# Kernel tuning notes

Measured on AMD Instinct MI355X. Metric: run time of the kernel, lower is better.

The kernel has to match this reference:

```python
import jax, jax.numpy as jnp
import numpy as np

N, D, E = 100000, 128, 1600000
BN_EPS = 1e-5

def setup_inputs() -> dict:
    key = jax.random.key(0)
    k1, k2, k3 = jax.random.split(key, 3)
    src_embeddings = jax.random.normal(k1, (N, D), dtype=jnp.float32)
    dst_embeddings = jax.random.normal(k2, (N, D), dtype=jnp.float32)
    graph = jax.random.randint(k3, (2, E), 0, N, dtype=jnp.int64)
    bn_weight = jnp.ones((1,), dtype=jnp.float32)
    bn_bias = jnp.zeros((1,), dtype=jnp.float32)
    return {
        "src_embeddings": src_embeddings,
        "dst_embeddings": dst_embeddings,
        "graph": graph,
        "bn_weight": bn_weight,
        "bn_bias": bn_bias,
    }

def reference(src_embeddings, dst_embeddings, graph, bn_weight, bn_bias):
    # gather endpoint embeddings by edge indices: [E, D]
    src = src_embeddings[graph[0]]
    dst = dst_embeddings[graph[1]]
    # squared distance per edge, clamped as in torch .clamp(min=1e-12)
    d2 = jnp.clip(jnp.sum((src - dst) ** 2, axis=-1), 1e-12, None)  # [E]
    likelihood = -jnp.log(d2)
    # BatchNorm1d(1) in training mode: batch mean, biased variance, eps=1e-5
    mu = jnp.mean(likelihood)
    var = jnp.mean((likelihood - mu) ** 2)
    edge_weights_logits = bn_weight[0] * (likelihood - mu) * jax.lax.rsqrt(var + BN_EPS) + bn_bias[0]
    # weighting_function = torch.sigmoid
    edge_weights = jax.nn.sigmoid(edge_weights_logits)
    # normalize=True: divide by mean
    edge_weights = edge_weights / jnp.mean(edge_weights)
    edge_weights = edge_weights[:, None]  # [E, 1]
    return graph, edge_weights, edge_weights_logits
```

## Files before the change

### kernel.cpp

```cpp
#include <hip/hip_runtime.h>
#include <math.h>

#define EMB_D 128
#define BN_EPS 1e-5f
#define GATHER_BLOCKS 2048
#define OVF_CAP 8192

typedef float v2f __attribute__((ext_vector_type(2)));

#if defined(__has_builtin)
#if __has_builtin(__builtin_amdgcn_cvt_pk_f32_fp8) && __has_builtin(__builtin_amdgcn_cvt_pk_fp8_f32)
#define FP8_HW 1
#endif
#endif

__device__ __forceinline__ unsigned int sw_f32_to_fp8(float x) {
    unsigned int u = __float_as_uint(x);
    unsigned int s = u >> 31;
    int e = (int)((u >> 23) & 0xff) - 127;
    unsigned int m = u & 0x7fffff;
    m += 0x7FFFF + ((m >> 20) & 1);
    if (m >> 23) { m = 0; e += 1; }
    int e8 = e + 7;
    if (e8 <= 0) return s << 7;
    if (e8 >= 15) return (s << 7) | 0x7E;
    return (s << 7) | ((unsigned)e8 << 3) | (m >> 20);
}

__device__ __forceinline__ float sw_fp8_to_f32(unsigned int v) {
    unsigned int s = (v >> 7) & 1, e = (v >> 3) & 15, m = v & 7;
    if (e == 0) return 0.0f;
    unsigned int bits = (s << 31) | ((e - 7 + 127) << 23) | (m << 20);
    return __uint_as_float(bits);
}

__device__ __forceinline__ unsigned int pack4_fp8(float4 v) {
#ifdef FP8_HW
    unsigned int o = 0;
    o = (unsigned int)__builtin_amdgcn_cvt_pk_fp8_f32(v.x, v.y, (int)o, false);
    o = (unsigned int)__builtin_amdgcn_cvt_pk_fp8_f32(v.z, v.w, (int)o, true);
    return o;
#else
    return sw_f32_to_fp8(v.x) | (sw_f32_to_fp8(v.y) << 8) |
           (sw_f32_to_fp8(v.z) << 16) | (sw_f32_to_fp8(v.w) << 24);
#endif
}

__device__ __forceinline__ float fp8x4_d2(unsigned int ua, unsigned int ub) {
#ifdef FP8_HW
    v2f a0 = __builtin_amdgcn_cvt_pk_f32_fp8((int)ua, false);
    v2f a1 = __builtin_amdgcn_cvt_pk_f32_fp8((int)ua, true);
    v2f b0 = __builtin_amdgcn_cvt_pk_f32_fp8((int)ub, false);
    v2f b1 = __builtin_amdgcn_cvt_pk_f32_fp8((int)ub, true);
    float dx = a0.x - b0.x, dy = a0.y - b0.y;
    float dz = a1.x - b1.x, dw = a1.y - b1.y;
#else
    float dx = sw_fp8_to_f32(ua & 0xff)         - sw_fp8_to_f32(ub & 0xff);
    float dy = sw_fp8_to_f32((ua >> 8) & 0xff)  - sw_fp8_to_f32((ub >> 8) & 0xff);
    float dz = sw_fp8_to_f32((ua >> 16) & 0xff) - sw_fp8_to_f32((ub >> 16) & 0xff);
    float dw = sw_fp8_to_f32(ua >> 24)          - sw_fp8_to_f32(ub >> 24);
#endif
    return fmaf(dx, dx, fmaf(dy, dy, fmaf(dz, dz, dw * dw)));
}

__device__ __forceinline__ float chunk_d2(uint4 a, uint4 b) {
    return fp8x4_d2(a.x, b.x) + fp8x4_d2(a.y, b.y)
         + fp8x4_d2(a.z, b.z) + fp8x4_d2(a.w, b.w);
}

__device__ __forceinline__ float edge_L(const unsigned char* src8,
                                        const unsigned char* dst8,
                                        int s, int d, int sub) {
    const uint4* sa = (const uint4*)(src8 + (long long)s * 128) + sub * 4;
    const uint4* sb = (const uint4*)(dst8 + (long long)d * 128) + sub * 4;
    const uint4 a0 = sa[0], a1 = sa[1], a2 = sa[2], a3 = sa[3];
    const uint4 b0 = sb[0], b1 = sb[1], b2 = sb[2], b3 = sb[3];
    float p = chunk_d2(a0, b0) + chunk_d2(a1, b1)
            + chunk_d2(a2, b2) + chunk_d2(a3, b3);
    p += __shfl_xor(p, 1, 64);
    return -logf(fmaxf(p, 1e-12f));
}

__global__ void prep_kernel(const float* __restrict__ src,
                            const float* __restrict__ dst,
                            unsigned int* __restrict__ src8,
                            unsigned int* __restrict__ dst8,
                            long long nElem,
                            double* __restrict__ acc,
                            unsigned int* __restrict__ cursors,
                            unsigned int cap)
{
    if (blockIdx.x == 0) {
        if (threadIdx.x < 65) cursors[threadIdx.x] = threadIdx.x * cap;
        if (threadIdx.x >= 65 && threadIdx.x < 68) acc[threadIdx.x - 65] = 0.0;
    }
    const long long nthreads = (long long)gridDim.x * blockDim.x;
    const long long tid0 = (long long)blockIdx.x * blockDim.x + threadIdx.x;
    const long long nvec = nElem / 4;
    for (long long i = tid0; i < nvec; i += nthreads)
        src8[i] = pack4_fp8(((const float4*)src)[i]);
    for (long long i = tid0; i < nvec; i += nthreads)
        dst8[i] = pack4_fp8(((const float4*)dst)[i]);
}

__global__ void bin_kernel(const int* __restrict__ g,
                           long long E,
                           unsigned long long* __restrict__ rec,
                           unsigned int* __restrict__ cursors,
                           unsigned int cap,
                           float inv_slice)
{
    __shared__ unsigned int hist[64];
    __shared__ unsigned int curs[64];

    const long long chunkSz = (long long)blockDim.x * 8;
    const long long nchunks = (E + chunkSz - 1) / chunkSz;

    for (long long c = blockIdx.x; c < nchunks; c += gridDim.x) {
        const long long base = c * chunkSz;
        if (threadIdx.x < 64) hist[threadIdx.x] = 0;
        __syncthreads();

        int bb[8];
        unsigned long long pk[8];
        #pragma unroll
        for (int k = 0; k < 8; ++k) {
            const long long e = base + (long long)k * blockDim.x + threadIdx.x;
            bb[k] = -1;
            if (e < E) {
                const unsigned int s = (unsigned int)g[e];
                const unsigned int d = (unsigned int)g[E + e];
                int bs = (int)((float)s * inv_slice); bs = bs > 7 ? 7 : bs;
                int bd = (int)((float)d * inv_slice); bd = bd > 7 ? 7 : bd;
                bb[k] = bs * 8 + bd;
                pk[k] = (unsigned long long)s | ((unsigned long long)d << 20)
                      | ((unsigned long long)e << 40);
                atomicAdd(&hist[bb[k]], 1u);
            }
        }
        __syncthreads();
        if (threadIdx.x < 64 && hist[threadIdx.x] > 0)
            curs[threadIdx.x] = atomicAdd(&cursors[threadIdx.x], hist[threadIdx.x]);
        __syncthreads();

        #pragma unroll
        for (int k = 0; k < 8; ++k) {
            if (bb[k] >= 0) {
                unsigned int off = atomicAdd(&curs[bb[k]], 1u);
                const unsigned int lim = (unsigned int)(bb[k] + 1) * cap;
                if (off < lim) {
                    rec[off] = pk[k];
                } else {
                    unsigned int oo = atomicAdd(&cursors[64], 1u);
                    if (oo < 64u * cap + OVF_CAP) rec[oo] = pk[k];
                }
            }
        }
        __syncthreads();
    }
}

__global__ void edge_l_binned_kernel(const unsigned char* __restrict__ src8,
                                     const unsigned char* __restrict__ dst8,
                                     const unsigned long long* __restrict__ rec,
                                     const unsigned int* __restrict__ cursors,
                                     unsigned int cap,
                                     float* __restrict__ l_out,
                                     double* __restrict__ acc)
{
    const int sub = threadIdx.x & 1;
    const int eg  = threadIdx.x >> 1;
    const int xcd = blockIdx.x & 7;
    const int local = blockIdx.x >> 3;
    const unsigned int perXcd = gridDim.x >> 3;
    const unsigned int stride = perXcd * 128;

    double sumL = 0.0, sumL2 = 0.0;

    for (int j = 0; j < 8; ++j) {
        const int b = xcd * 8 + j;
        const unsigned int start = (unsigned int)b * cap;
        unsigned int end = cursors[b];
        const unsigned int lim = (unsigned int)(b + 1) * cap;
        if (end > lim) end = lim;
        for (unsigned int idx = start + (unsigned int)local * 128u + eg;
             idx < end; idx += stride) {
            const unsigned long long v = rec[idx];
            const int s = (int)(v & 0xFFFFFu);
            const int d = (int)((v >> 20) & 0xFFFFFu);
            const long long eid = (long long)(v >> 40);
            const float L = edge_L(src8, dst8, s, d, sub);
            if (sub == 0) {
                l_out[eid] = L;
                sumL  += (double)L;
                sumL2 += (double)L * (double)L;
            }
        }
    }

    {
        const unsigned int start = 64u * cap;
        unsigned int end = cursors[64];
        if (end > start + OVF_CAP) end = start + OVF_CAP;
        const unsigned int gstride = gridDim.x * 128u;
        for (unsigned int idx = start + blockIdx.x * 128u + eg;
             idx < end; idx += gstride) {
            const unsigned long long v = rec[idx];
            const int s = (int)(v & 0xFFFFFu);
            const int d = (int)((v >> 20) & 0xFFFFFu);
            const long long eid = (long long)(v >> 40);
            const float L = edge_L(src8, dst8, s, d, sub);
            if (sub == 0) {
                l_out[eid] = L;
                sumL  += (double)L;
                sumL2 += (double)L * (double)L;
            }
        }
    }

    __shared__ double sA[256];
    __shared__ double sB[256];
    sA[threadIdx.x] = sumL;
    sB[threadIdx.x] = sumL2;
    __syncthreads();
    for (int ofs = 128; ofs >= 1; ofs >>= 1) {
        if ((int)threadIdx.x < ofs) {
            sA[threadIdx.x] += sA[threadIdx.x + ofs];
            sB[threadIdx.x] += sB[threadIdx.x + ofs];
        }
        __syncthreads();
    }
    if (threadIdx.x == 0) {
        atomicAdd(&acc[0], sA[0]);
        atomicAdd(&acc[1], sB[0]);
    }
}

__global__ void edge_l_fp8_kernel(const unsigned char* __restrict__ src8,
                                  const unsigned char* __restrict__ dst8,
                                  const int* __restrict__ g,
                                  long long E,
                                  float*  __restrict__ l_out,
                                  double* __restrict__ acc)
{
    const int sub = threadIdx.x & 1;
    const int eg  = threadIdx.x >> 1;
    const long long stride = (long long)gridDim.x * 128;

    double sumL = 0.0, sumL2 = 0.0;

    long long e = (long long)blockIdx.x * 128 + eg;
    int s = 0, d = 0;
    if (e < E) { s = g[e]; d = g[E + e]; }

    while (e < E) {
        const long long en = e + stride;
        int sn = 0, dn = 0;
        if (en < E) { sn = g[en]; dn = g[E + en]; }
        const float L = edge_L(src8, dst8, s, d, sub);
        if (sub == 0) {
            l_out[e] = L;
            sumL  += (double)L;
            sumL2 += (double)L * (double)L;
        }
        e = en; s = sn; d = dn;
    }

    __shared__ double sA[256];
    __shared__ double sB[256];
    sA[threadIdx.x] = sumL;
    sB[threadIdx.x] = sumL2;
    __syncthreads();
    for (int ofs = 128; ofs >= 1; ofs >>= 1) {
        if ((int)threadIdx.x < ofs) {
            sA[threadIdx.x] += sA[threadIdx.x + ofs];
            sB[threadIdx.x] += sB[threadIdx.x + ofs];
        }
        __syncthreads();
    }
    if (threadIdx.x == 0) {
        atomicAdd(&acc[0], sA[0]);
        atomicAdd(&acc[1], sB[0]);
    }
}

__global__ void edge_l_kernel(const float* __restrict__ src,
                              const float* __restrict__ dst,
                              const int*   __restrict__ g,
                              long long E,
                              float*  __restrict__ l_out,
                              double* __restrict__ acc)
{
    const int sub  = threadIdx.x & 7;
    const int egrp = threadIdx.x >> 3;
    const long long stride = (long long)gridDim.x * 32;

    double sumL = 0.0, sumL2 = 0.0;

    long long e = (long long)blockIdx.x * 32 + egrp;
    int s = 0, d = 0;
    if (e < E) { s = g[e]; d = g[E + e]; }

    while (e < E) {
        const long long en = e + stride;
        int sn = 0, dn = 0;
        if (en < E) { sn = g[en]; dn = g[E + en]; }

        const float4* sa = (const float4*)(src + (long long)s * EMB_D);
        const float4* sb = (const float4*)(dst + (long long)d * EMB_D);
        const float4 a0 = sa[sub];      const float4 b0 = sb[sub];
        const float4 a1 = sa[sub + 8];  const float4 b1 = sb[sub + 8];
        const float4 a2 = sa[sub + 16]; const float4 b2 = sb[sub + 16];
        const float4 a3 = sa[sub + 24]; const float4 b3 = sb[sub + 24];

        float dx, dy, dz, dw, p = 0.f;
        dx = a0.x-b0.x; dy = a0.y-b0.y; dz = a0.z-b0.z; dw = a0.w-b0.w;
        p += fmaf(dx,dx,fmaf(dy,dy,fmaf(dz,dz,dw*dw)));
        dx = a1.x-b1.x; dy = a1.y-b1.y; dz = a1.z-b1.z; dw = a1.w-b1.w;
        p += fmaf(dx,dx,fmaf(dy,dy,fmaf(dz,dz,dw*dw)));
        dx = a2.x-b2.x; dy = a2.y-b2.y; dz = a2.z-b2.z; dw = a2.w-b2.w;
        p += fmaf(dx,dx,fmaf(dy,dy,fmaf(dz,dz,dw*dw)));
        dx = a3.x-b3.x; dy = a3.y-b3.y; dz = a3.z-b3.z; dw = a3.w-b3.w;
        p += fmaf(dx,dx,fmaf(dy,dy,fmaf(dz,dz,dw*dw)));

        p += __shfl_xor(p, 1, 64);
        p += __shfl_xor(p, 2, 64);
        p += __shfl_xor(p, 4, 64);

        if (sub == 0) {
            const float L = -logf(fmaxf(p, 1e-12f));
            l_out[e] = L;
            sumL  += (double)L;
            sumL2 += (double)L * (double)L;
        }
        e = en; s = sn; d = dn;
    }

    __shared__ double sA[256];
    __shared__ double sB[256];
    sA[threadIdx.x] = sumL;
    sB[threadIdx.x] = sumL2;
    __syncthreads();
    for (int ofs = 128; ofs >= 1; ofs >>= 1) {
        if ((int)threadIdx.x < ofs) {
            sA[threadIdx.x] += sA[threadIdx.x + ofs];
            sB[threadIdx.x] += sB[threadIdx.x + ofs];
        }
        __syncthreads();
    }
    if (threadIdx.x == 0) {
        atomicAdd(&acc[0], sA[0]);
        atomicAdd(&acc[1], sB[0]);
    }
}

__global__ void bn_sig_kernel(float* __restrict__ logits,
                              float* __restrict__ ew,
                              const double* __restrict__ acc,
                              double* __restrict__ sig_acc,
                              const float* __restrict__ bn_w,
                              const float* __restrict__ bn_b,
                              long long E)
{
    const long long nthreads = (long long)gridDim.x * blockDim.x;
    const long long tid0 = (long long)blockIdx.x * blockDim.x + threadIdx.x;

    __shared__ float s_mu, s_inv, s_w, s_b;
    if (threadIdx.x == 0) {
        const double mu  = acc[0] / (double)E;
        const double var = acc[1] / (double)E - mu * mu;
        s_mu  = (float)mu;
        s_inv = (float)(1.0 / sqrt(var + (double)BN_EPS));
        s_w   = bn_w[0];
        s_b   = bn_b[0];
    }
    __syncthreads();
    const float mu = s_mu, inv = s_inv, w = s_w, b = s_b;

    double sig = 0.0;
    for (long long i = tid0; i < E; i += nthreads) {
        const float L = logits[i];
        const float z = w * (L - mu) * inv + b;
        logits[i] = z;
        const float sg = 1.0f / (1.0f + expf(-z));
        ew[i] = sg;
        sig += (double)sg;
    }

    __shared__ double sS[256];
    sS[threadIdx.x] = sig;
    __syncthreads();
    for (int ofs = 128; ofs >= 1; ofs >>= 1) {
        if ((int)threadIdx.x < ofs)
            sS[threadIdx.x] += sS[threadIdx.x + ofs];
        __syncthreads();
    }
    if (threadIdx.x == 0)
        atomicAdd(sig_acc, sS[0]);
}

__global__ void norm_graph_kernel(float* __restrict__ ew,
                                  const double* __restrict__ sig_acc,
                                  const int* __restrict__ g,
                                  float* __restrict__ out_graph,
                                  long long E)
{
    const long long nthreads = (long long)gridDim.x * blockDim.x;
    const long long tid0 = (long long)blockIdx.x * blockDim.x + threadIdx.x;
    const float scale = (float)((double)E / sig_acc[0]);

    const long long nvec = E / 4;
    for (long long i = tid0; i < nvec; i += nthreads) {
        float4 v = ((float4*)ew)[i];
        v.x *= scale; v.y *= scale; v.z *= scale; v.w *= scale;
        ((float4*)ew)[i] = v;
    }
    for (long long i = nvec * 4 + tid0; i < E; i += nthreads)
        ew[i] *= scale;

    const long long gvec = (2 * E) / 4;
    for (long long i = tid0; i < gvec; i += nthreads) {
        const int4 v = ((const int4*)g)[i];
        float4 f;
        f.x = (float)v.x; f.y = (float)v.y; f.z = (float)v.z; f.w = (float)v.w;
        ((float4*)out_graph)[i] = f;
    }
    for (long long i = gvec * 4 + tid0; i < 2 * E; i += nthreads)
        out_graph[i] = (float)g[i];
}

extern "C" void kernel_launch(void* const* d_in, const int* in_sizes, int n_in,
                              void* d_out, int out_size, void* d_ws, size_t ws_size,
                              hipStream_t stream) {
    const float* src  = (const float*)d_in[0];
    const float* dst  = (const float*)d_in[1];
    const int*   g    = (const int*)d_in[2];
    const float* bn_w = (const float*)d_in[3];
    const float* bn_b = (const float*)d_in[4];

    const long long N = (long long)in_sizes[0] / EMB_D;
    const long long E = (long long)in_sizes[2] / 2;

    float* out        = (float*)d_out;
    float* out_graph  = out;
    float* out_ew     = out + 2 * E;
    float* out_logits = out + 3 * E;

    double*       acc     = (double*)d_ws;
    unsigned int* cursors = (unsigned int*)((char*)d_ws + 64);
    unsigned char* src8   = (unsigned char*)d_ws + 512;
    unsigned char* dst8   = src8 + (size_t)N * EMB_D;
    unsigned long long* rec = (unsigned long long*)(dst8 + (size_t)N * EMB_D);

    const unsigned int cap = (unsigned int)(E / 64 + 2048);
    const size_t need_full = 512 + (size_t)N * EMB_D * 2
                           + ((size_t)64 * cap + OVF_CAP) * 8;
    const size_t need_fp8  = 512 + (size_t)N * EMB_D * 2;

    const int slice_sz = (int)((N + 7) / 8);
    const float inv_slice = 1.0f / (float)slice_sz;

    if (ws_size >= need_full && N < (1 << 20) && E < (1LL << 24)) {
        prep_kernel<<<4096, 256, 0, stream>>>(src, dst,
                                              (unsigned int*)src8,
                                              (unsigned int*)dst8,
                                              N * EMB_D, acc, cursors, cap);
        bin_kernel<<<1024, 256, 0, stream>>>(g, E, rec, cursors, cap, inv_slice);
        edge_l_binned_kernel<<<GATHER_BLOCKS, 256, 0, stream>>>(
            src8, dst8, rec, cursors, cap, out_logits, acc);
    } else if (ws_size >= need_fp8) {
        prep_kernel<<<4096, 256, 0, stream>>>(src, dst,
                                              (unsigned int*)src8,
                                              (unsigned int*)dst8,
                                              N * EMB_D, acc, cursors, cap);
        edge_l_fp8_kernel<<<4096, 256, 0, stream>>>(src8, dst8, g, E,
                                                    out_logits, acc);
    } else {
        hipMemsetAsync(d_ws, 0, 3 * sizeof(double), stream);
        edge_l_kernel<<<4096, 256, 0, stream>>>(src, dst, g, E, out_logits, acc);
    }

    bn_sig_kernel<<<2048, 256, 0, stream>>>(out_logits, out_ew, acc, &acc[2],
                                            bn_w, bn_b, E);
    norm_graph_kernel<<<2048, 256, 0, stream>>>(out_ew, &acc[2], g, out_graph, E);
}
```

Baseline: 293.8 us.

## Fuse prep with binning, regroup gather to 8 lanes, vectorize BN pass

Merges the fp8 table conversion and the edge binning into one kernel that also writes the float graph output, so the norm kernel skips the graph copy. Bin cursors become relative counts and are zeroed by a memset instead of in-kernel initialization. The gather kernel walks each XCD's bins through a single flat index, uses 8 lanes per edge with two edges in flight per lane group, and writes logits with nontemporal stores. The BN/sigmoid pass is vectorized with float4, and grid sizes for the tail kernels are halved. The gain in parallelism and fewer launches comes with a prefix lookup per record, and the fused prep kernel depends on the binning grid being suitable for the conversion loop.

```diff
diff --git a/kernel.cpp b/kernel.cpp
--- a/kernel.cpp
+++ b/kernel.cpp
@@ -81,35 +81,42 @@
     return -logf(fmaxf(p, 1e-12f));
 }
 
-__global__ void prep_kernel(const float* __restrict__ src,
-                            const float* __restrict__ dst,
-                            unsigned int* __restrict__ src8,
-                            unsigned int* __restrict__ dst8,
-                            long long nElem,
-                            double* __restrict__ acc,
-                            unsigned int* __restrict__ cursors,
-                            unsigned int cap)
-{
-    if (blockIdx.x == 0) {
-        if (threadIdx.x < 65) cursors[threadIdx.x] = threadIdx.x * cap;
-        if (threadIdx.x >= 65 && threadIdx.x < 68) acc[threadIdx.x - 65] = 0.0;
-    }
-    const long long nthreads = (long long)gridDim.x * blockDim.x;
-    const long long tid0 = (long long)blockIdx.x * blockDim.x + threadIdx.x;
-    const long long nvec = nElem / 4;
-    for (long long i = tid0; i < nvec; i += nthreads)
-        src8[i] = pack4_fp8(((const float4*)src)[i]);
-    for (long long i = tid0; i < nvec; i += nthreads)
-        dst8[i] = pack4_fp8(((const float4*)dst)[i]);
-}
-
-__global__ void bin_kernel(const int* __restrict__ g,
-                           long long E,
-                           unsigned long long* __restrict__ rec,
-                           unsigned int* __restrict__ cursors,
-                           unsigned int cap,
-                           float inv_slice)
-{
+__device__ __forceinline__ unsigned int flat_to_rec(unsigned int f,
+                                                    const unsigned int (&pre)[9],
+                                                    unsigned int cap) {
+    unsigned int j = 0, pj = 0;
+    #pragma unroll
+    for (int k = 1; k < 8; ++k) {
+        const bool ge = (f >= pre[k]);
+        j  = ge ? (unsigned int)k : j;
+        pj = ge ? pre[k] : pj;
+    }
+    return j * cap + (f - pj);
+}
+
+__global__ void prep_bin_kernel(const float* __restrict__ src,
+                                const float* __restrict__ dst,
+                                unsigned int* __restrict__ src8,
+                                unsigned int* __restrict__ dst8,
+                                long long nElem,
+                                const int* __restrict__ g,
+                                long long E,
+                                float* __restrict__ out_graph,
+                                unsigned long long* __restrict__ rec,
+                                unsigned int* __restrict__ cursors,
+                                unsigned int cap,
+                                float inv_slice)
+{
+    {
+        const long long nthreads = (long long)gridDim.x * blockDim.x;
+        const long long tid0 = (long long)blockIdx.x * blockDim.x + threadIdx.x;
+        const long long nvec = nElem / 4;
+        for (long long i = tid0; i < nvec; i += nthreads)
+            src8[i] = pack4_fp8(((const float4*)src)[i]);
+        for (long long i = tid0; i < nvec; i += nthreads)
+            dst8[i] = pack4_fp8(((const float4*)dst)[i]);
+    }
+
     __shared__ unsigned int hist[64];
     __shared__ unsigned int curs[64];
 
@@ -130,6 +137,8 @@
             if (e < E) {
                 const unsigned int s = (unsigned int)g[e];
                 const unsigned int d = (unsigned int)g[E + e];
+                out_graph[e]     = (float)s;
+                out_graph[E + e] = (float)d;
                 int bs = (int)((float)s * inv_slice); bs = bs > 7 ? 7 : bs;
                 int bd = (int)((float)d * inv_slice); bd = bd > 7 ? 7 : bd;
                 bb[k] = bs * 8 + bd;
@@ -147,12 +156,11 @@
         for (int k = 0; k < 8; ++k) {
             if (bb[k] >= 0) {
                 unsigned int off = atomicAdd(&curs[bb[k]], 1u);
-                const unsigned int lim = (unsigned int)(bb[k] + 1) * cap;
-                if (off < lim) {
-                    rec[off] = pk[k];
+                if (off < cap) {
+                    rec[(unsigned int)bb[k] * cap + off] = pk[k];
                 } else {
                     unsigned int oo = atomicAdd(&cursors[64], 1u);
-                    if (oo < 64u * cap + OVF_CAP) rec[oo] = pk[k];
+                    if (oo < OVF_CAP) rec[64u * cap + oo] = pk[k];
                 }
             }
         }
@@ -160,62 +168,169 @@
     }
 }
 
-__global__ void edge_l_binned_kernel(const unsigned char* __restrict__ src8,
-                                     const unsigned char* __restrict__ dst8,
-                                     const unsigned long long* __restrict__ rec,
-                                     const unsigned int* __restrict__ cursors,
-                                     unsigned int cap,
-                                     float* __restrict__ l_out,
-                                     double* __restrict__ acc)
-{
-    const int sub = threadIdx.x & 1;
-    const int eg  = threadIdx.x >> 1;
+__global__ void edge_l_binned2_kernel(const unsigned char* __restrict__ src8,
+                                      const unsigned char* __restrict__ dst8,
+                                      const unsigned long long* __restrict__ rec,
+                                      const unsigned int* __restrict__ cursors,
+                                      unsigned int cap,
+                                      float* __restrict__ l_out,
+                                      double* __restrict__ acc)
+{
+    const int tid = threadIdx.x;
+    const int sub = tid & 7;
+    const int grp = tid >> 3;
     const int xcd = blockIdx.x & 7;
-    const int local = blockIdx.x >> 3;
-    const unsigned int perXcd = gridDim.x >> 3;
-    const unsigned int stride = perXcd * 128;
+    const unsigned int local = blockIdx.x >> 3;
+    const unsigned int nloc  = gridDim.x >> 3;
+
+    unsigned int pre[9];
+    pre[0] = 0;
+    #pragma unroll
+    for (int j = 0; j < 8; ++j) {
+        unsigned int c = cursors[xcd * 8 + j];
+        if (c > cap) c = cap;
+        pre[j + 1] = pre[j] + c;
+    }
+    const unsigned int M = pre[8];
+    const unsigned long long recBase = (unsigned long long)(xcd * 8) * cap;
 
     double sumL = 0.0, sumL2 = 0.0;
 
-    for (int j = 0; j < 8; ++j) {
-        const int b = xcd * 8 + j;
-        const unsigned int start = (unsigned int)b * cap;
-        unsigned int end = cursors[b];
-        const unsigned int lim = (unsigned int)(b + 1) * cap;
-        if (end > lim) end = lim;
-        for (unsigned int idx = start + (unsigned int)local * 128u + eg;
-             idx < end; idx += stride) {
-            const unsigned long long v = rec[idx];
-            const int s = (int)(v & 0xFFFFFu);
-            const int d = (int)((v >> 20) & 0xFFFFFu);
-            const long long eid = (long long)(v >> 40);
-            const float L = edge_L(src8, dst8, s, d, sub);
-            if (sub == 0) {
-                l_out[eid] = L;
+    const unsigned int perBlock = 64;
+    const unsigned int stride = nloc * perBlock;
+
+    for (unsigned int f0 = local * perBlock; f0 < M; f0 += stride) {
+        const unsigned int f1 = f0 + (unsigned int)grp;
+        const unsigned int f2 = f1 + 32u;
+        const bool ok1 = f1 < M;
+        const bool ok2 = f2 < M;
+
+        unsigned long long v1 = 0ull, v2 = 0ull;
+        if (ok1) v1 = rec[recBase + flat_to_rec(f1, pre, cap)];
+        if (ok2) v2 = rec[recBase + flat_to_rec(f2, pre, cap)];
+
+        const int s1 = (int)(v1 & 0xFFFFFu);
+        const int d1 = (int)((v1 >> 20) & 0xFFFFFu);
+        const int s2 = (int)(v2 & 0xFFFFFu);
+        const int d2i = (int)((v2 >> 20) & 0xFFFFFu);
+
+        const uint4 A1 = ((const uint4*)(src8 + (long long)s1 * 128))[sub];
+        const uint4 B1 = ((const uint4*)(dst8 + (long long)d1 * 128))[sub];
+        const uint4 A2 = ((const uint4*)(src8 + (long long)s2 * 128))[sub];
+        const uint4 B2 = ((const uint4*)(dst8 + (long long)d2i * 128))[sub];
+
+        float p1 = chunk_d2(A1, B1);
+        float p2 = chunk_d2(A2, B2);
+
+        p1 += __shfl_xor(p1, 1, 64);
+        p1 += __shfl_xor(p1, 2, 64);
+        p1 += __shfl_xor(p1, 4, 64);
+        p2 += __shfl_xor(p2, 1, 64);
+        p2 += __shfl_xor(p2, 2, 64);
+        p2 += __shfl_xor(p2, 4, 64);
+
+        if (sub == 0) {
+            if (ok1) {
+                const float L = -logf(fmaxf(p1, 1e-12f));
+                __builtin_nontemporal_store(L, &l_out[(long long)(v1 >> 40)]);
                 sumL  += (double)L;
                 sumL2 += (double)L * (double)L;
             }
-        }
-    }
-
-    {
-        const unsigned int start = 64u * cap;
-        unsigned int end = cursors[64];
-        if (end > start + OVF_CAP) end = start + OVF_CAP;
-        const unsigned int gstride = gridDim.x * 128u;
-        for (unsigned int idx = start + blockIdx.x * 128u + eg;
-             idx < end; idx += gstride) {
-            const unsigned long long v = rec[idx];
-            const int s = (int)(v & 0xFFFFFu);
-            const int d = (int)((v >> 20) & 0xFFFFFu);
-            const long long eid = (long long)(v >> 40);
-            const float L = edge_L(src8, dst8, s, d, sub);
-            if (sub == 0) {
-                l_out[eid] = L;
+            if (ok2) {
+                const float L = -logf(fmaxf(p2, 1e-12f));
+                __builtin_nontemporal_store(L, &l_out[(long long)(v2 >> 40)]);
                 sumL  += (double)L;
                 sumL2 += (double)L * (double)L;
             }
         }
+    }
+
+    {
+        unsigned int ovfN = cursors[64];
+        if (ovfN > OVF_CAP) ovfN = OVF_CAP;
+        const unsigned long long obase = 64ull * cap;
+        const unsigned int gstride = gridDim.x * 32u;
+        for (unsigned int f = blockIdx.x * 32u + (unsigned int)grp;
+             f < ovfN; f += gstride) {
+            const unsigned long long v = rec[obase + f];
+            const int s = (int)(v & 0xFFFFFu);
+            const int d = (int)((v >> 20) & 0xFFFFFu);
+            const uint4 A = ((const uint4*)(src8 + (long long)s * 128))[sub];
+            const uint4 B = ((const uint4*)(dst8 + (long long)d * 128))[sub];
+            float p = chunk_d2(A, B);
+            p += __shfl_xor(p, 1, 64);
+            p += __shfl_xor(p, 2, 64);
+            p += __shfl_xor(p, 4, 64);
+            if (sub == 0) {
+                const float L = -logf(fmaxf(p, 1e-12f));
+                __builtin_nontemporal_store(L, &l_out[(long long)(v >> 40)]);
+                sumL  += (double)L;
+                sumL2 += (double)L * (double)L;
+            }
+        }
+    }
+
+    __shared__ double sA[256];
+    __shared__ double sB[256];
+    sA[tid] = sumL;
+    sB[tid] = sumL2;
+    __syncthreads();
+    for (int ofs = 128; ofs >= 1; ofs >>= 1) {
+        if (tid < ofs) {
+            sA[tid] += sA[tid + ofs];
+            sB[tid] += sB[tid + ofs];
+        }
+        __syncthreads();
+    }
+    if (tid == 0) {
+        atomicAdd(&acc[0], sA[0]);
+        atomicAdd(&acc[1], sB[0]);
+    }
+}
+
+__global__ void prep_tables_kernel(const float* __restrict__ src,
+                                   const float* __restrict__ dst,
+                                   unsigned int* __restrict__ src8,
+                                   unsigned int* __restrict__ dst8,
+                                   long long nElem)
+{
+    const long long nthreads = (long long)gridDim.x * blockDim.x;
+    const long long tid0 = (long long)blockIdx.x * blockDim.x + threadIdx.x;
+    const long long nvec = nElem / 4;
+    for (long long i = tid0; i < nvec; i += nthreads)
+        src8[i] = pack4_fp8(((const float4*)src)[i]);
+    for (long long i = tid0; i < nvec; i += nthreads)
+        dst8[i] = pack4_fp8(((const float4*)dst)[i]);
+}
+
+__global__ void edge_l_fp8_kernel(const unsigned char* __restrict__ src8,
+                                  const unsigned char* __restrict__ dst8,
+                                  const int* __restrict__ g,
+                                  long long E,
+                                  float*  __restrict__ l_out,
+                                  double* __restrict__ acc)
+{
+    const int sub = threadIdx.x & 1;
+    const int eg  = threadIdx.x >> 1;
+    const long long stride = (long long)gridDim.x * 128;
+
+    double sumL = 0.0, sumL2 = 0.0;
+
+    long long e = (long long)blockIdx.x * 128 + eg;
+    int s = 0, d = 0;
+    if (e < E) { s = g[e]; d = g[E + e]; }
+
+    while (e < E) {
+        const long long en = e + stride;
+        int sn = 0, dn = 0;
+        if (en < E) { sn = g[en]; dn = g[E + en]; }
+        const float L = edge_L(src8, dst8, s, d, sub);
+        if (sub == 0) {
+            l_out[e] = L;
+            sumL  += (double)L;
+            sumL2 += (double)L * (double)L;
+        }
+        e = en; s = sn; d = dn;
     }
 
     __shared__ double sA[256];
@@ -236,20 +351,20 @@
     }
 }
 
-__global__ void edge_l_fp8_kernel(const unsigned char* __restrict__ src8,
-                                  const unsigned char* __restrict__ dst8,
-                                  const int* __restrict__ g,
-                                  long long E,
-                                  float*  __restrict__ l_out,
-                                  double* __restrict__ acc)
-{
-    const int sub = threadIdx.x & 1;
-    const int eg  = threadIdx.x >> 1;
-    const long long stride = (long long)gridDim.x * 128;
+__global__ void edge_l_kernel(const float* __restrict__ src,
+                              const float* __restrict__ dst,
+                              const int*   __restrict__ g,
+                              long long E,
+                              float*  __restrict__ l_out,
+                              double* __restrict__ acc)
+{
+    const int sub  = threadIdx.x & 7;
+    const int egrp = threadIdx.x >> 3;
+    const long long stride = (long long)gridDim.x * 32;
 
     double sumL = 0.0, sumL2 = 0.0;
 
-    long long e = (long long)blockIdx.x * 128 + eg;
+    long long e = (long long)blockIdx.x * 32 + egrp;
     int s = 0, d = 0;
     if (e < E) { s = g[e]; d = g[E + e]; }
 
@@ -257,8 +372,30 @@
         const long long en = e + stride;
         int sn = 0, dn = 0;
         if (en < E) { sn = g[en]; dn = g[E + en]; }
-        const float L = edge_L(src8, dst8, s, d, sub);
+
+        const float4* sa = (const float4*)(src + (long long)s * EMB_D);
+        const float4* sb = (const float4*)(dst + (long long)d * EMB_D);
+        const float4 a0 = sa[sub];      const float4 b0 = sb[sub];
+        const float4 a1 = sa[sub + 8];  const float4 b1 = sb[sub + 8];
+        const float4 a2 = sa[sub + 16]; const float4 b2 = sb[sub + 16];
+        const float4 a3 = sa[sub + 24]; const float4 b3 = sb[sub + 24];
+
+        float dx, dy, dz, dw, p = 0.f;
+        dx = a0.x-b0.x; dy = a0.y-b0.y; dz = a0.z-b0.z; dw = a0.w-b0.w;
+        p += fmaf(dx,dx,fmaf(dy,dy,fmaf(dz,dz,dw*dw)));
+        dx = a1.x-b1.x; dy = a1.y-b1.y; dz = a1.z-b1.z; dw = a1.w-b1.w;
+        p += fmaf(dx,dx,fmaf(dy,dy,fmaf(dz,dz,dw*dw)));
+        dx = a2.x-b2.x; dy = a2.y-b2.y; dz = a2.z-b2.z; dw = a2.w-b2.w;
+        p += fmaf(dx,dx,fmaf(dy,dy,fmaf(dz,dz,dw*dw)));
+        dx = a3.x-b3.x; dy = a3.y-b3.y; dz = a3.z-b3.z; dw = a3.w-b3.w;
+        p += fmaf(dx,dx,fmaf(dy,dy,fmaf(dz,dz,dw*dw)));
+
+        p += __shfl_xor(p, 1, 64);
+        p += __shfl_xor(p, 2, 64);
+        p += __shfl_xor(p, 4, 64);
+
         if (sub == 0) {
+            const float L = -logf(fmaxf(p, 1e-12f));
             l_out[e] = L;
             sumL  += (double)L;
             sumL2 += (double)L * (double)L;
@@ -284,76 +421,6 @@
     }
 }
 
-__global__ void edge_l_kernel(const float* __restrict__ src,
-                              const float* __restrict__ dst,
-                              const int*   __restrict__ g,
-                              long long E,
-                              float*  __restrict__ l_out,
-                              double* __restrict__ acc)
-{
-    const int sub  = threadIdx.x & 7;
-    const int egrp = threadIdx.x >> 3;
-    const long long stride = (long long)gridDim.x * 32;
-
-    double sumL = 0.0, sumL2 = 0.0;
-
-    long long e = (long long)blockIdx.x * 32 + egrp;
-    int s = 0, d = 0;
-    if (e < E) { s = g[e]; d = g[E + e]; }
-
-    while (e < E) {
-        const long long en = e + stride;
-        int sn = 0, dn = 0;
-        if (en < E) { sn = g[en]; dn = g[E + en]; }
-
-        const float4* sa = (const float4*)(src + (long long)s * EMB_D);
-        const float4* sb = (const float4*)(dst + (long long)d * EMB_D);
-        const float4 a0 = sa[sub];      const float4 b0 = sb[sub];
-        const float4 a1 = sa[sub + 8];  const float4 b1 = sb[sub + 8];
-        const float4 a2 = sa[sub + 16]; const float4 b2 = sb[sub + 16];
-        const float4 a3 = sa[sub + 24]; const float4 b3 = sb[sub + 24];
-
-        float dx, dy, dz, dw, p = 0.f;
-        dx = a0.x-b0.x; dy = a0.y-b0.y; dz = a0.z-b0.z; dw = a0.w-b0.w;
-        p += fmaf(dx,dx,fmaf(dy,dy,fmaf(dz,dz,dw*dw)));
-        dx = a1.x-b1.x; dy = a1.y-b1.y; dz = a1.z-b1.z; dw = a1.w-b1.w;
-        p += fmaf(dx,dx,fmaf(dy,dy,fmaf(dz,dz,dw*dw)));
-        dx = a2.x-b2.x; dy = a2.y-b2.y; dz = a2.z-b2.z; dw = a2.w-b2.w;
-        p += fmaf(dx,dx,fmaf(dy,dy,fmaf(dz,dz,dw*dw)));
-        dx = a3.x-b3.x; dy = a3.y-b3.y; dz = a3.z-b3.z; dw = a3.w-b3.w;
-        p += fmaf(dx,dx,fmaf(dy,dy,fmaf(dz,dz,dw*dw)));
-
-        p += __shfl_xor(p, 1, 64);
-        p += __shfl_xor(p, 2, 64);
-        p += __shfl_xor(p, 4, 64);
-
-        if (sub == 0) {
-            const float L = -logf(fmaxf(p, 1e-12f));
-            l_out[e] = L;
-            sumL  += (double)L;
-            sumL2 += (double)L * (double)L;
-        }
-        e = en; s = sn; d = dn;
-    }
-
-    __shared__ double sA[256];
-    __shared__ double sB[256];
-    sA[threadIdx.x] = sumL;
-    sB[threadIdx.x] = sumL2;
-    __syncthreads();
-    for (int ofs = 128; ofs >= 1; ofs >>= 1) {
-        if ((int)threadIdx.x < ofs) {
-            sA[threadIdx.x] += sA[threadIdx.x + ofs];
-            sB[threadIdx.x] += sB[threadIdx.x + ofs];
-        }
-        __syncthreads();
-    }
-    if (threadIdx.x == 0) {
-        atomicAdd(&acc[0], sA[0]);
-        atomicAdd(&acc[1], sB[0]);
-    }
-}
-
 __global__ void bn_sig_kernel(float* __restrict__ logits,
                               float* __restrict__ ew,
                               const double* __restrict__ acc,
@@ -378,7 +445,24 @@
     const float mu = s_mu, inv = s_inv, w = s_w, b = s_b;
 
     double sig = 0.0;
-    for (long long i = tid0; i < E; i += nthreads) {
+    const long long nvec = E / 4;
+    for (long long i = tid0; i < nvec; i += nthreads) {
+        float4 L = ((const float4*)logits)[i];
+        float4 z;
+        z.x = w * (L.x - mu) * inv + b;
+        z.y = w * (L.y - mu) * inv + b;
+        z.z = w * (L.z - mu) * inv + b;
+        z.w = w * (L.w - mu) * inv + b;
+        ((float4*)logits)[i] = z;
+        float4 sg;
+        sg.x = 1.0f / (1.0f + expf(-z.x));
+        sg.y = 1.0f / (1.0f + expf(-z.y));
+        sg.z = 1.0f / (1.0f + expf(-z.z));
+        sg.w = 1.0f / (1.0f + expf(-z.w));
+        ((float4*)ew)[i] = sg;
+        sig += (double)(sg.x + sg.y) + (double)(sg.z + sg.w);
+    }
+    for (long long i = nvec * 4 + tid0; i < E; i += nthreads) {
         const float L = logits[i];
         const float z = w * (L - mu) * inv + b;
         logits[i] = z;
@@ -399,11 +483,12 @@
         atomicAdd(sig_acc, sS[0]);
 }
 
-__global__ void norm_graph_kernel(float* __restrict__ ew,
-                                  const double* __restrict__ sig_acc,
-                                  const int* __restrict__ g,
-                                  float* __restrict__ out_graph,
-                                  long long E)
+__global__ void norm_kernel(float* __restrict__ ew,
+                            const double* __restrict__ sig_acc,
+                            const int* __restrict__ g,
+                            float* __restrict__ out_graph,
+                            int do_graph,
+                            long long E)
 {
     const long long nthreads = (long long)gridDim.x * blockDim.x;
     const long long tid0 = (long long)blockIdx.x * blockDim.x + threadIdx.x;
@@ -411,22 +496,24 @@
 
     const long long nvec = E / 4;
     for (long long i = tid0; i < nvec; i += nthreads) {
-        float4 v = ((float4*)ew)[i];
+        float4 v = ((const float4*)ew)[i];
         v.x *= scale; v.y *= scale; v.z *= scale; v.w *= scale;
         ((float4*)ew)[i] = v;
     }
     for (long long i = nvec * 4 + tid0; i < E; i += nthreads)
         ew[i] *= scale;
 
-    const long long gvec = (2 * E) / 4;
-    for (long long i = tid0; i < gvec; i += nthreads) {
-        const int4 v = ((const int4*)g)[i];
-        float4 f;
-        f.x = (float)v.x; f.y = (float)v.y; f.z = (float)v.z; f.w = (float)v.w;
-        ((float4*)out_graph)[i] = f;
-    }
-    for (long long i = gvec * 4 + tid0; i < 2 * E; i += nthreads)
-        out_graph[i] = (float)g[i];
+    if (do_graph) {
+        const long long gvec = (2 * E) / 4;
+        for (long long i = tid0; i < gvec; i += nthreads) {
+            const int4 v = ((const int4*)g)[i];
+            float4 f;
+            f.x = (float)v.x; f.y = (float)v.y; f.z = (float)v.z; f.w = (float)v.w;
+            ((float4*)out_graph)[i] = f;
+        }
+        for (long long i = gvec * 4 + tid0; i < 2 * E; i += nthreads)
+            out_graph[i] = (float)g[i];
+    }
 }
 
 extern "C" void kernel_launch(void* const* d_in, const int* in_sizes, int n_in,
@@ -460,27 +547,33 @@
     const int slice_sz = (int)((N + 7) / 8);
     const float inv_slice = 1.0f / (float)slice_sz;
 
+    hipMemsetAsync(d_ws, 0, 512, stream);
+
     if (ws_size >= need_full && N < (1 << 20) && E < (1LL << 24)) {
-        prep_kernel<<<4096, 256, 0, stream>>>(src, dst,
-                                              (unsigned int*)src8,
-                                              (unsigned int*)dst8,
-                                              N * EMB_D, acc, cursors, cap);
-        bin_kernel<<<1024, 256, 0, stream>>>(g, E, rec, cursors, cap, inv_slice);
-        edge_l_binned_kernel<<<GATHER_BLOCKS, 256, 0, stream>>>(
+        prep_bin_kernel<<<4096, 256, 0, stream>>>(src, dst,
+                                                  (unsigned int*)src8,
+                                                  (unsigned int*)dst8,
+                                                  N * EMB_D, g, E, out_graph,
+                                                  rec, cursors, cap, inv_slice);
+        edge_l_binned2_kernel<<<GATHER_BLOCKS, 256, 0, stream>>>(
             src8, dst8, rec, cursors, cap, out_logits, acc);
+        bn_sig_kernel<<<1024, 256, 0, stream>>>(out_logits, out_ew, acc, &acc[2],
+                                                bn_w, bn_b, E);
+        norm_kernel<<<1024, 256, 0, stream>>>(out_ew, &acc[2], g, out_graph, 0, E);
     } else if (ws_size >= need_fp8) {
-        prep_kernel<<<4096, 256, 0, stream>>>(src, dst,
-                                              (unsigned int*)src8,
-                                              (unsigned int*)dst8,
-                                              N * EMB_D, acc, cursors, cap);
+        prep_tables_kernel<<<4096, 256, 0, stream>>>(src, dst,
+                                                     (unsigned int*)src8,
+                                                     (unsigned int*)dst8,
+                                                     N * EMB_D);
         edge_l_fp8_kernel<<<4096, 256, 0, stream>>>(src8, dst8, g, E,
                                                     out_logits, acc);
+        bn_sig_kernel<<<1024, 256, 0, stream>>>(out_logits, out_ew, acc, &acc[2],
+                                                bn_w, bn_b, E);
+        norm_kernel<<<1024, 256, 0, stream>>>(out_ew, &acc[2], g, out_graph, 1, E);
     } else {
-        hipMemsetAsync(d_ws, 0, 3 * sizeof(double), stream);
         edge_l_kernel<<<4096, 256, 0, stream>>>(src, dst, g, E, out_logits, acc);
-    }
-
-    bn_sig_kernel<<<2048, 256, 0, stream>>>(out_logits, out_ew, acc, &acc[2],
-                                            bn_w, bn_b, E);
-    norm_graph_kernel<<<2048, 256, 0, stream>>>(out_ew, &acc[2], g, out_graph, E);
-}
+        bn_sig_kernel<<<1024, 256, 0, stream>>>(out_logits, out_ew, acc, &acc[2],
+                                                bn_w, bn_b, E);
+        norm_kernel<<<1024, 256, 0, stream>>>(out_ew, &acc[2], g, out_graph, 1, E);
+    }
+}
```

New measurement: 262.6 us. 1.12x faster.
